# Kernel optimization log

Measured on AMD Instinct MI355X. Metric: run time of the kernel, lower is better.

The kernel has to match this reference:

```python
import jax, jax.numpy as jnp
import numpy as np

B, N, K = 2, 8192, 16
D_IN, D_OUT = 32, 128
EPS = 1e-5


def _bn(x, gamma, beta):
    # x: (B, C, L); BatchNorm1d training-mode stats over (B, L)
    mean = x.mean(axis=(0, 2), keepdims=True)
    var = x.var(axis=(0, 2), keepdims=True)
    return gamma[None, :, None] * (x - mean) * jax.lax.rsqrt(var + EPS) + beta[None, :, None]


def _shared_mlp(x, w, b, gamma, beta, act):
    # SharedMLP: 1x1 Conv1d (channel GEMM) + BN + activation. x: (B, Cin, L)
    y = jnp.einsum('oi,bil->bol', w, x) + b[None, :, None]
    return act(_bn(y, gamma, beta))


def _attentive_pool(x, w, b):
    # x: (B, C, N, K); per-(b,n,k) Linear over C, softmax over K, weighted sum over K
    scores = jnp.einsum('oc,bcnk->bonk', w, x) + b[None, :, None, None]
    scores = jax.nn.softmax(scores, axis=-1)
    return jnp.sum(scores * x, axis=-1)  # (B, C, N)  (torch keeps K=1 dim; squeezed by SharedMLP reshape)


def _knn(coords, k):
    # brute-force squared-L2 KNN excluding self (faiss IndexFlatL2 semantics)
    sq = jnp.sum(coords * coords, axis=-1)  # (B, N)
    d2 = sq[:, :, None] + sq[:, None, :] - 2.0 * jnp.einsum('bid,bjd->bij', coords, coords)
    n = coords.shape[1]
    d2 = jnp.where(jnp.eye(n, dtype=bool)[None], jnp.inf, d2)
    neg, idx = jax.lax.top_k(-d2, k)  # ascending squared distance
    return idx, jnp.maximum(-neg, 0.0)


def _lse(coords, features, idx, dist, w, b, gamma, beta):
    # LocalSpatialEncoding: gather neighbor coords, build 10-ch relative features, MLP, concat
    Bq, Nq, Kq = idx.shape
    neighbor = jax.vmap(lambda c, i: c[i])(coords, idx)  # (B, N, K, 3)
    center = jnp.broadcast_to(coords[:, :, None, :], neighbor.shape)
    rel = center - neighbor
    spatial = jnp.concatenate([center, neighbor, rel, dist[..., None]], axis=-1)  # (B, N, K, 10)
    spatial = spatial.transpose(0, 3, 1, 2).reshape(Bq, 10, Nq * Kq)
    sf = _shared_mlp(spatial, w, b, gamma, beta, jax.nn.relu).reshape(Bq, -1, Nq, Kq)
    feat = jnp.broadcast_to(features[..., None], (Bq, features.shape[1], Nq, Kq))
    return jnp.concatenate([sf, feat], axis=1)


def _forward(coords, features,
             mlp1_w, mlp1_b, mlp1_g, mlp1_bt,
             lse1_w, lse1_b, lse1_g, lse1_bt,
             mlpp1_w, mlpp1_b, mlpp1_g, mlpp1_bt,
             lse2_w, lse2_b, lse2_g, lse2_bt,
             mlp2_w, mlp2_b, mlp2_g, mlp2_bt,
             res_w, res_b, res_g, res_bt,
             pool1_w, pool1_b, pool2_w, pool2_b):
    # faiss output is detached in torch (numpy round-trip) -> stop_gradient
    idx, dist = _knn(jax.lax.stop_gradient(coords), K)
    lrelu02 = lambda v: jnp.where(v >= 0, v, 0.2 * v)   # LeakyReLU(0.2)
    lrelu01 = lambda v: jnp.where(v >= 0, v, 0.01 * v)  # default LeakyReLU
    x = _shared_mlp(features, mlp1_w, mlp1_b, mlp1_g, mlp1_bt, lrelu02)      # (B, 64, N)
    x = _lse(coords, x, idx, dist, lse1_w, lse1_b, lse1_g, lse1_bt)          # (B, 128, N, K)
    x = _attentive_pool(x, pool1_w, pool1_b)                                  # (B, 128, N)
    x = _shared_mlp(x, mlpp1_w, mlpp1_b, mlpp1_g, mlpp1_bt, jax.nn.relu)     # (B, 32, N)
    x = _lse(coords, x, idx, dist, lse2_w, lse2_b, lse2_g, lse2_bt)          # (B, 64, N, K)
    x = _attentive_pool(x, pool2_w, pool2_b)                                  # (B, 64, N)
    x_main = _shared_mlp(x, mlp2_w, mlp2_b, mlp2_g, mlp2_bt, jax.nn.relu)    # (B, 128, N)
    resid = _shared_mlp(features, res_w, res_b, res_g, res_bt, jax.nn.relu)  # (B, 128, N)
    return lrelu01(jnp.concatenate([x_main, resid], axis=1))                 # (B, 256, N)


def setup_inputs() -> dict:
    key = jax.random.key(0)
    ks = iter(jax.random.split(key, 64))

    def lin(ci, co):
        w = jax.random.normal(next(ks), (co, ci), jnp.float32) / np.float32(np.sqrt(ci))
        b = jax.random.normal(next(ks), (co,), jnp.float32) * 0.01
        return w, b

    inp = {}
    inp['coords'] = jax.random.normal(next(ks), (B, N, 3), jnp.float32)
    inp['features'] = jax.random.normal(next(ks), (B, D_IN, N), jnp.float32)
    for name, ci, co in [('mlp1', D_IN, D_OUT // 2), ('lse1', 10, D_OUT // 2),
                         ('mlpp1', D_OUT, D_OUT // 4), ('lse2', 10, D_OUT // 4),
                         ('mlp2', D_OUT // 2, D_OUT), ('res', D_IN, D_OUT)]:
        w, b = lin(ci, co)
        inp[name + '_w'], inp[name + '_b'] = w, b
        inp[name + '_g'] = jnp.ones((co,), jnp.float32)
        inp[name + '_bt'] = jnp.zeros((co,), jnp.float32)
    for name, c in [('pool1', D_OUT), ('pool2', D_OUT // 2)]:
        w, b = lin(c, c)
        inp[name + '_w'], inp[name + '_b'] = w, b
    return inp


def reference(coords, features,
              mlp1_w, mlp1_b, mlp1_g, mlp1_bt,
              lse1_w, lse1_b, lse1_g, lse1_bt,
              mlpp1_w, mlpp1_b, mlpp1_g, mlpp1_bt,
              lse2_w, lse2_b, lse2_g, lse2_bt,
              mlp2_w, mlp2_b, mlp2_g, mlp2_bt,
              res_w, res_b, res_g, res_bt,
              pool1_w, pool1_b, pool2_w, pool2_b):
    return _forward(coords, features,
                    mlp1_w, mlp1_b, mlp1_g, mlp1_bt,
                    lse1_w, lse1_b, lse1_g, lse1_bt,
                    mlpp1_w, mlpp1_b, mlpp1_g, mlpp1_bt,
                    lse2_w, lse2_b, lse2_g, lse2_bt,
                    mlp2_w, mlp2_b, mlp2_g, mlp2_bt,
                    res_w, res_b, res_g, res_bt,
                    pool1_w, pool1_b, pool2_w, pool2_b)
```

## Files before the change

kernel.cpp:

```cpp
#include <hip/hip_runtime.h>

static constexpr int N_ = 8192;
static constexpr int B_ = 2;
static constexpr int K_ = 16;

typedef __attribute__((ext_vector_type(8))) short bf16x8;
typedef __attribute__((ext_vector_type(4))) float f32x4;

__device__ __forceinline__ short f2bf(float f) {
  unsigned int u = __float_as_uint(f);
  unsigned int r = (u + 0x7FFFu + ((u >> 16) & 1u)) >> 16;
  return (short)r;
}
__device__ __forceinline__ float bf2f(short h) {
  return __uint_as_float(((unsigned int)(unsigned short)h) << 16);
}
__device__ __forceinline__ float dpp_shr1_f(float x) {
  return __uint_as_float((unsigned int)__builtin_amdgcn_update_dpp(
      0, (int)__float_as_uint(x), 0x111, 0xF, 0xF, true));
}
__device__ __forceinline__ int dpp_shr1_i(int x) {
  return __builtin_amdgcn_update_dpp(0, x, 0x111, 0xF, 0xF, true);
}
__device__ __forceinline__ float rdlane_f(float x, int l) {
  return __uint_as_float(__builtin_amdgcn_readlane(__float_as_uint(x), l));
}

__global__ __launch_bounds__(512) void knn_kernel(const float* __restrict__ coords,
                                                  int* __restrict__ oidx,
                                                  float* __restrict__ odist) {
  __shared__ float4 pts[2048];
  const int b = blockIdx.y;
  const int wv = threadIdx.x >> 6;
  const int lane = threadIdx.x & 63;
  const bool lpos = (lane != 0);
  const int q0 = blockIdx.x * 16 + wv * 2;
  const int q1 = q0 + 1;
  const float* cb = coords + (size_t)b * N_ * 3;
  const float qx0 = cb[q0 * 3 + 0], qy0 = cb[q0 * 3 + 1], qz0 = cb[q0 * 3 + 2];
  const float qx1 = cb[q1 * 3 + 0], qy1 = cb[q1 * 3 + 1], qz1 = cb[q1 * 3 + 2];
  const float qsq0 = __fadd_rn(__fadd_rn(__fmul_rn(qx0, qx0), __fmul_rn(qy0, qy0)), __fmul_rn(qz0, qz0));
  const float qsq1 = __fadd_rn(__fadd_rn(__fmul_rn(qx1, qx1), __fmul_rn(qy1, qy1)), __fmul_rn(qz1, qz1));
  float kd0 = INFINITY, kd1 = INFINITY;
  int ki0 = 0, ki1 = 0;
  float tau0 = INFINITY, tau1 = INFINITY;
  for (int t0 = 0; t0 < N_; t0 += 2048) {
    __syncthreads();
    for (int i = threadIdx.x; i < 2048; i += 512) {
      const int p = t0 + i;
      const float x = cb[p * 3 + 0], y = cb[p * 3 + 1], z = cb[p * 3 + 2];
      const float sq = __fadd_rn(__fadd_rn(__fmul_rn(x, x), __fmul_rn(y, y)), __fmul_rn(z, z));
      pts[i] = make_float4(x, y, z, sq);
    }
    __syncthreads();
    for (int s = 0; s < 2048; s += 64) {
      const float4 p = pts[s + lane];
      const int base = t0 + s;
      float d20, d21;
      {
        const float dot = __fadd_rn(__fadd_rn(__fmul_rn(qx0, p.x), __fmul_rn(qy0, p.y)), __fmul_rn(qz0, p.z));
        d20 = __fsub_rn(__fadd_rn(qsq0, p.w), __fmul_rn(2.0f, dot));
      }
      {
        const float dot = __fadd_rn(__fadd_rn(__fmul_rn(qx1, p.x), __fmul_rn(qy1, p.y)), __fmul_rn(qz1, p.z));
        d21 = __fsub_rn(__fadd_rn(qsq1, p.w), __fmul_rn(2.0f, dot));
      }
      unsigned long long m0 = __ballot(d20 < tau0);
      unsigned long long m1 = __ballot(d21 < tau1);
      if (base == (q0 & ~63)) m0 &= ~(1ull << (q0 & 63));
      if (base == (q1 & ~63)) m1 &= ~(1ull << (q1 & 63));
      while (m0) {
        const int src = __builtin_ctzll(m0);
        const float dc = rdlane_f(d20, src);
        const int jc = base + src;
        const float sd = dpp_shr1_f(kd0);
        const int si = dpp_shr1_i(ki0);
        const bool c1 = kd0 > dc;
        const bool c2 = lpos && (sd > dc);
        kd0 = c1 ? (c2 ? sd : dc) : kd0;
        ki0 = c1 ? (c2 ? si : jc) : ki0;
        m0 &= (m0 - 1);
        tau0 = rdlane_f(kd0, 15);
        m0 &= __ballot(d20 < tau0);
      }
      while (m1) {
        const int src = __builtin_ctzll(m1);
        const float dc = rdlane_f(d21, src);
        const int jc = base + src;
        const float sd = dpp_shr1_f(kd1);
        const int si = dpp_shr1_i(ki1);
        const bool c1 = kd1 > dc;
        const bool c2 = lpos && (sd > dc);
        kd1 = c1 ? (c2 ? sd : dc) : kd1;
        ki1 = c1 ? (c2 ? si : jc) : ki1;
        m1 &= (m1 - 1);
        tau1 = rdlane_f(kd1, 15);
        m1 &= __ballot(d21 < tau1);
      }
    }
  }
  if (lane < 16) {
    oidx[((size_t)b * N_ + q0) * K_ + lane] = ki0;
    odist[((size_t)b * N_ + q0) * K_ + lane] = fmaxf(kd0, 0.0f);
    oidx[((size_t)b * N_ + q1) * K_ + lane] = ki1;
    odist[((size_t)b * N_ + q1) * K_ + lane] = fmaxf(kd1, 0.0f);
  }
}

__device__ __forceinline__ float snn_get(const float* SNN, int a, int b) {
  const int i = a < b ? a : b, j = a < b ? b : a;
  return SNN[i == 0 ? j : (i == 1 ? 2 + j : 3 + j)];
}
__device__ __forceinline__ float mom_mean(int i, const float* C, const float* SN, float Sd) {
  if (i < 3) return 16.0f * C[i];
  if (i < 6) return SN[i - 3];
  if (i < 9) return 16.0f * C[i - 6] - SN[i - 6];
  return Sd;
}
__device__ __forceinline__ float mom_prod(int i, int j, const float* C, const float* SN,
                                          const float* SNN, float Sd, float Sdd, const float* SND) {
  const int ti = i < 3 ? 0 : (i < 6 ? 1 : (i < 9 ? 2 : 3));
  const int tj = j < 3 ? 0 : (j < 6 ? 1 : (j < 9 ? 2 : 3));
  const int a = (ti == 3) ? 0 : (i - ti * 3);
  const int bb = (tj == 3) ? 0 : (j - tj * 3);
  if (ti == 0 && tj == 0) return 16.0f * C[a] * C[bb];
  if (ti == 0 && tj == 1) return C[a] * SN[bb];
  if (ti == 0 && tj == 2) return C[a] * (16.0f * C[bb] - SN[bb]);
  if (ti == 0 && tj == 3) return C[a] * Sd;
  if (ti == 1 && tj == 1) return snn_get(SNN, a, bb);
  if (ti == 1 && tj == 2) return C[bb] * SN[a] - snn_get(SNN, a, bb);
  if (ti == 1 && tj == 3) return SND[a];
  if (ti == 2 && tj == 2) return 16.0f * C[a] * C[bb] - C[a] * SN[bb] - C[bb] * SN[a] + snn_get(SNN, a, bb);
  if (ti == 2 && tj == 3) return C[a] * Sd - SND[a];
  return Sdd;
}

__global__ __launch_bounds__(64) void moments_kernel(const float* __restrict__ coords,
                                                     const int* __restrict__ knn_i,
                                                     const float* __restrict__ knn_d,
                                                     double* __restrict__ mom) {
  const int t = blockIdx.x * 64 + threadIdx.x;
  const int b = t >> 13, n = t & (N_ - 1);
  const float* cb = coords + (size_t)b * N_ * 3;
  float C[3] = {cb[n * 3 + 0], cb[n * 3 + 1], cb[n * 3 + 2]};
  float SN[3] = {0.f, 0.f, 0.f}, SNN[6] = {0.f, 0.f, 0.f, 0.f, 0.f, 0.f};
  float SND[3] = {0.f, 0.f, 0.f}, Sd = 0.f, Sdd = 0.f;
  for (int k = 0; k < K_; ++k) {
    const int id = knn_i[(size_t)t * K_ + k];
    const float dd = knn_d[(size_t)t * K_ + k];
    const float nx = cb[id * 3 + 0], ny = cb[id * 3 + 1], nz = cb[id * 3 + 2];
    SN[0] += nx; SN[1] += ny; SN[2] += nz;
    SNN[0] += nx * nx; SNN[1] += nx * ny; SNN[2] += nx * nz;
    SNN[3] += ny * ny; SNN[4] += ny * nz; SNN[5] += nz * nz;
    Sd += dd; Sdd += dd * dd;
    SND[0] += nx * dd; SND[1] += ny * dd; SND[2] += nz * dd;
  }
  float m65[65];
  int e = 0;
#pragma unroll
  for (int i = 0; i < 10; ++i) m65[e++] = mom_mean(i, C, SN, Sd);
#pragma unroll
  for (int i = 0; i < 10; ++i)
#pragma unroll
    for (int j = i; j < 10; ++j) m65[e++] = mom_prod(i, j, C, SN, SNN, Sd, Sdd, SND);
#pragma unroll
  for (int q = 0; q < 65; ++q) {
    float v = m65[q];
#pragma unroll
    for (int off = 32; off > 0; off >>= 1) v += __shfl_xor(v, off);
    m65[q] = v;
  }
  __shared__ float buf[65];
  if (threadIdx.x == 0) {
#pragma unroll
    for (int q = 0; q < 65; ++q) buf[q] = m65[q];
  }
  __syncthreads();
  if (threadIdx.x < 64) atomicAdd(&mom[threadIdx.x], (double)buf[threadIdx.x]);
  if (threadIdx.x == 0) atomicAdd(&mom[64], (double)buf[64]);
}

template <int CI, int CO>
__device__ __forceinline__ void conv_frag_seg(const float* __restrict__ w, short* __restrict__ H,
                                              short* __restrict__ L, int tid, int nthr) {
  constexpr int NT = CO / 16;
  for (int i = tid; i < CI * CO; i += nthr) {
    const int j = i & 7, l = (i >> 3) & 63, tmp = i >> 9;
    const int tt = tmp % NT, cc = tmp / NT;
    const int c = cc * 32 + (l >> 4) * 8 + j;
    const int o = tt * 16 + (l & 15);
    const float v = w[o * CI + c];
    const short h = f2bf(v);
    H[i] = h;
    L[i] = f2bf(v - bf2f(h));
  }
}

__global__ __launch_bounds__(256) void convert_kernel(
    const float* __restrict__ pw1, const float* __restrict__ pw2,
    short* __restrict__ wB1, short* __restrict__ wB2,
    const float* __restrict__ wm1, short* __restrict__ f1H, short* __restrict__ f1L,
    const float* __restrict__ wmp, short* __restrict__ f2H, short* __restrict__ f2L,
    const float* __restrict__ wm2, short* __restrict__ f3H, short* __restrict__ f3L,
    const float* __restrict__ wrs, short* __restrict__ fRH, short* __restrict__ fRL) {
  const int blk = blockIdx.x;
  if (blk < 8) {
    const int tid = blk * 256 + threadIdx.x;
    for (int i = tid; i < 128 * 128; i += 2048) wB1[i] = f2bf(pw1[i]);
  } else if (blk < 10) {
    const int tid = (blk - 8) * 256 + threadIdx.x;
    for (int i = tid; i < 64 * 64; i += 512) wB2[i] = f2bf(pw2[i]);
  } else if (blk < 12) {
    conv_frag_seg<32, 64>(wm1, f1H, f1L, (blk - 10) * 256 + threadIdx.x, 512);
  } else if (blk < 16) {
    conv_frag_seg<128, 32>(wmp, f2H, f2L, (blk - 12) * 256 + threadIdx.x, 1024);
  } else if (blk < 24) {
    conv_frag_seg<64, 128>(wm2, f3H, f3L, (blk - 16) * 256 + threadIdx.x, 2048);
  } else {
    conv_frag_seg<32, 128>(wrs, fRH, fRL, (blk - 24) * 256 + threadIdx.x, 1024);
  }
}

__global__ void setup_kernel(const double* __restrict__ mom,
                             const float* __restrict__ w1, const float* __restrict__ b1,
                             const float* __restrict__ g1, const float* __restrict__ t1,
                             const float* __restrict__ w2, const float* __restrict__ b2,
                             const float* __restrict__ g2, const float* __restrict__ t2,
                             float* __restrict__ w1f, float* __restrict__ b1f,
                             float* __restrict__ w2f, float* __restrict__ b2f) {
  const int t = threadIdx.x;
  __shared__ double mu[10];
  __shared__ double S[10][10];
  const double cnt = (double)B_ * N_ * K_;
  if (t < 10) mu[t] = mom[t] / cnt;
  if (t < 55) {
    int e = t, i = 0;
    while (e >= 10 - i) { e -= 10 - i; ++i; }
    const int j = i + e;
    const double v = mom[10 + t] / cnt;
    S[i][j] = v;
    S[j][i] = v;
  }
  __syncthreads();
  const float *w, *bias, *gg, *bt;
  float *wf, *bf;
  int c;
  if (t < 64) { w = w1; bias = b1; gg = g1; bt = t1; wf = w1f; bf = b1f; c = t; }
  else if (t < 96) { w = w2; bias = b2; gg = g2; bt = t2; wf = w2f; bf = b2f; c = t - 64; }
  else return;
  double wd[10];
#pragma unroll
  for (int d = 0; d < 10; ++d) wd[d] = (double)w[c * 10 + d];
  const double cbv = (double)bias[c];
  double mz = cbv;
  for (int d = 0; d < 10; ++d) mz += wd[d] * mu[d];
  double e2 = cbv * cbv;
  for (int d = 0; d < 10; ++d) e2 += 2.0 * cbv * wd[d] * mu[d];
  for (int d = 0; d < 10; ++d)
    for (int e = 0; e < 10; ++e) e2 += wd[d] * wd[e] * S[d][e];
  const double var = e2 - mz * mz;
  const double a = (double)gg[c] / sqrt(var + 1e-5);
  const double shift = (double)bt[c] - a * mz;
#pragma unroll
  for (int d = 0; d < 10; ++d) wf[c * 10 + d] = (float)(a * wd[d]);
  bf[c] = (float)(a * cbv + shift);
}

template <int CI, int CO, bool ROWMAJ>
__global__ __launch_bounds__(256) void gemm_mfma_kernel(const float* __restrict__ in,
                                                        const short* __restrict__ fragH,
                                                        const short* __restrict__ fragL,
                                                        const float* __restrict__ bias,
                                                        float* __restrict__ out,
                                                        double* __restrict__ sacc) {
  constexpr int NT = CO / 16;
  constexpr int NC = CI / 32;
  __shared__ float part[4][CO][2];
  const int wv = threadIdx.x >> 6, l = threadIdx.x & 63;
  const int col = l & 15, quad = l >> 4;
  const int p0 = blockIdx.x * 64 + wv * 16;
  const int pt = p0 + col;
  f32x4 d[NT];
#pragma unroll
  for (int t = 0; t < NT; ++t) {
    const float bv = bias[t * 16 + col];
    d[t][0] = bv; d[t][1] = bv; d[t][2] = bv; d[t][3] = bv;
  }
#pragma unroll
  for (int cc = 0; cc < NC; ++cc) {
    float xv[8];
    if (ROWMAJ) {
      const float* ip = in + (size_t)pt * CI + cc * 32 + quad * 8;
      *(float4*)&xv[0] = *(const float4*)ip;
      *(float4*)&xv[4] = *(const float4*)(ip + 4);
    } else {
      const int b = pt >> 13, n = pt & (N_ - 1);
      const float* ip = in + ((size_t)b * CI + cc * 32 + quad * 8) * N_ + n;
#pragma unroll
      for (int j = 0; j < 8; ++j) xv[j] = ip[(size_t)j * N_];
    }
    union { bf16x8 v; short u[8]; } AH, AL;
#pragma unroll
    for (int j = 0; j < 8; ++j) {
      const short h = f2bf(xv[j]);
      AH.u[j] = h;
      AL.u[j] = f2bf(xv[j] - bf2f(h));
    }
#pragma unroll
    for (int t = 0; t < NT; ++t) {
      const size_t fo = ((size_t)(cc * NT + t) * 64 + l) * 8;
      const bf16x8 BH = *(const bf16x8*)(fragH + fo);
      const bf16x8 BL = *(const bf16x8*)(fragL + fo);
      d[t] = __builtin_amdgcn_mfma_f32_16x16x32_bf16(AH.v, BH, d[t], 0, 0, 0);
      d[t] = __builtin_amdgcn_mfma_f32_16x16x32_bf16(AH.v, BL, d[t], 0, 0, 0);
      d[t] = __builtin_amdgcn_mfma_f32_16x16x32_bf16(AL.v, BH, d[t], 0, 0, 0);
    }
  }
#pragma unroll
  for (int t = 0; t < NT; ++t) {
#pragma unroll
    for (int r = 0; r < 4; ++r)
      out[(size_t)(p0 + quad * 4 + r) * CO + t * 16 + col] = d[t][r];
    float s1 = d[t][0] + d[t][1] + d[t][2] + d[t][3];
    float s2 = d[t][0] * d[t][0] + d[t][1] * d[t][1] + d[t][2] * d[t][2] + d[t][3] * d[t][3];
    s1 += __shfl_xor(s1, 16); s1 += __shfl_xor(s1, 32);
    s2 += __shfl_xor(s2, 16); s2 += __shfl_xor(s2, 32);
    if (quad == 0) { part[wv][t * 16 + col][0] = s1; part[wv][t * 16 + col][1] = s2; }
  }
  __syncthreads();
  if (threadIdx.x < CO) {
    const int o = threadIdx.x;
    atomicAdd(&sacc[o], (double)(part[0][o][0] + part[1][o][0] + part[2][o][0] + part[3][o][0]));
    atomicAdd(&sacc[CO + o], (double)(part[0][o][1] + part[1][o][1] + part[2][o][1] + part[3][o][1]));
  }
}

template <int CSF, int CF>
__global__ __launch_bounds__(256) void pool_kernel(
    const float* __restrict__ coords, const int* __restrict__ knn_i, const float* __restrict__ knn_d,
    const float* __restrict__ wlse, const float* __restrict__ blse,
    const float* __restrict__ feat, const double* __restrict__ sfe,
    const float* __restrict__ gfe, const float* __restrict__ tfe,
    const float slope,
    const short* __restrict__ wB, const float* __restrict__ pb,
    float* __restrict__ out) {
  constexpr int C = CSF + CF;
  constexpr int CP = C + 4;
  constexpr int NT = C / 16;
  constexpr int NC = C / 32;
  __shared__ float xcat[4][16][CP];
  __shared__ float sp[4][10][16];
  const int g = threadIdx.x >> 6;
  const int l = threadIdx.x & 63;
  const int quad = l >> 4, col = l & 15;
  const int pid = blockIdx.x * 4 + g;
  const int b = pid >> 13, n = pid & (N_ - 1);
  const float* cb = coords + (size_t)b * N_ * 3;

  if (l < 16) {
    const int id = knn_i[(size_t)pid * K_ + l];
    const float dd = knn_d[(size_t)pid * K_ + l];
    const float cx = cb[n * 3 + 0], cy = cb[n * 3 + 1], cz = cb[n * 3 + 2];
    const float nx = cb[id * 3 + 0], ny = cb[id * 3 + 1], nz = cb[id * 3 + 2];
    sp[g][0][l] = cx; sp[g][1][l] = cy; sp[g][2][l] = cz;
    sp[g][3][l] = nx; sp[g][4][l] = ny; sp[g][5][l] = nz;
    sp[g][6][l] = cx - nx; sp[g][7][l] = cy - ny; sp[g][8][l] = cz - nz;
    sp[g][9][l] = dd;
  }
  if (l < CF) {
    const double cnt = (double)(B_ * N_);
    const double mean = sfe[l] / cnt;
    const double var = sfe[CF + l] / cnt - mean * mean;
    const double av = (double)gfe[l] / sqrt(var + 1e-5);
    const float af = (float)av;
    const float bfv = (float)((double)tfe[l] - av * mean);
    float v = feat[(size_t)pid * CF + l];
    v = af * v + bfv;
    v = (v >= 0.0f) ? v : slope * v;
#pragma unroll
    for (int j = 0; j < 16; ++j) xcat[g][j][CSF + l] = v;
  }
  __syncthreads();
  if (l < CSF) {
    float z[16];
    const float bz = blse[l];
#pragma unroll
    for (int j = 0; j < 16; ++j) z[j] = bz;
#pragma unroll
    for (int d = 0; d < 10; ++d) {
      const float wv = wlse[l * 10 + d];
      const float4* sr = (const float4*)&sp[g][d][0];
      const float4 s0 = sr[0], s1 = sr[1], s2 = sr[2], s3 = sr[3];
      z[0] += wv * s0.x; z[1] += wv * s0.y; z[2] += wv * s0.z; z[3] += wv * s0.w;
      z[4] += wv * s1.x; z[5] += wv * s1.y; z[6] += wv * s1.z; z[7] += wv * s1.w;
      z[8] += wv * s2.x; z[9] += wv * s2.y; z[10] += wv * s2.z; z[11] += wv * s2.w;
      z[12] += wv * s3.x; z[13] += wv * s3.y; z[14] += wv * s3.z; z[15] += wv * s3.w;
    }
#pragma unroll
    for (int j = 0; j < 16; ++j) xcat[g][j][l] = fmaxf(z[j], 0.0f);
  }
  __syncthreads();
  f32x4 d[NT];
#pragma unroll
  for (int t = 0; t < NT; ++t) {
    const float pbv = pb[t * 16 + col];
    d[t][0] = pbv; d[t][1] = pbv; d[t][2] = pbv; d[t][3] = pbv;
  }
#pragma unroll
  for (int cc = 0; cc < NC; ++cc) {
    const float* xr = &xcat[g][col][cc * 32 + quad * 8];
    const float4 xa = *(const float4*)xr;
    const float4 xb = *(const float4*)(xr + 4);
    union { bf16x8 v; short u[8]; } A;
    A.u[0] = f2bf(xa.x); A.u[1] = f2bf(xa.y); A.u[2] = f2bf(xa.z); A.u[3] = f2bf(xa.w);
    A.u[4] = f2bf(xb.x); A.u[5] = f2bf(xb.y); A.u[6] = f2bf(xb.z); A.u[7] = f2bf(xb.w);
#pragma unroll
    for (int t = 0; t < NT; ++t) {
      const bf16x8 Bv = *(const bf16x8*)(wB + (size_t)(t * 16 + col) * C + cc * 32 + quad * 8);
      d[t] = __builtin_amdgcn_mfma_f32_16x16x32_bf16(A.v, Bv, d[t], 0, 0, 0);
    }
  }
#pragma unroll
  for (int t = 0; t < NT; ++t) {
    float mx = fmaxf(fmaxf(d[t][0], d[t][1]), fmaxf(d[t][2], d[t][3]));
    mx = fmaxf(mx, __shfl_xor(mx, 16));
    mx = fmaxf(mx, __shfl_xor(mx, 32));
    float e0 = __expf(d[t][0] - mx), e1 = __expf(d[t][1] - mx);
    float e2 = __expf(d[t][2] - mx), e3 = __expf(d[t][3] - mx);
    float s = e0 + e1 + e2 + e3;
    s += __shfl_xor(s, 16);
    s += __shfl_xor(s, 32);
    const int o = t * 16 + col;
    float part = e0 * xcat[g][quad * 4 + 0][o] + e1 * xcat[g][quad * 4 + 1][o] +
                 e2 * xcat[g][quad * 4 + 2][o] + e3 * xcat[g][quad * 4 + 3][o];
    part += __shfl_xor(part, 16);
    part += __shfl_xor(part, 32);
    if (quad == 0) out[(size_t)pid * C + o] = part / s;
  }
}

__global__ __launch_bounds__(256) void final_kernel(const float* __restrict__ y3,
                                                    const float* __restrict__ yr,
                                                    const double* __restrict__ s3,
                                                    const float* __restrict__ g3, const float* __restrict__ t3,
                                                    const double* __restrict__ sr,
                                                    const float* __restrict__ gr, const float* __restrict__ tr,
                                                    float* __restrict__ out) {
  __shared__ float tile[256 * 17];
  const int blk = blockIdx.x;
  const int b = blk >> 9;
  const int n0 = (blk & 511) << 4;
  const int c = threadIdx.x;
  const float* src;
  const double* sa;
  const float *gp, *tp;
  int cc;
  if (c < 128) { src = y3; sa = s3; gp = g3; tp = t3; cc = c; }
  else { src = yr; sa = sr; gp = gr; tp = tr; cc = c - 128; }
  const double cnt = (double)(B_ * N_);
  const double mean = sa[cc] / cnt;
  const double var = sa[128 + cc] / cnt - mean * mean;
  const double avd = (double)gp[cc] / sqrt(var + 1e-5);
  const float av = (float)avd;
  const float bv = (float)((double)tp[cc] - avd * mean);
#pragma unroll
  for (int nl = 0; nl < 16; ++nl) {
    const float x = av * src[((size_t)(b * N_ + n0 + nl)) * 128 + cc] + bv;
    tile[c * 17 + nl] = fmaxf(x, 0.0f);
  }
  __syncthreads();
  const int np = c & 15, grp = c >> 4;
#pragma unroll
  for (int j = 0; j < 16; ++j) {
    const int c2 = grp * 16 + j;
    out[((size_t)(b * 256 + c2)) * N_ + n0 + np] = tile[c2 * 17 + np];
  }
}

extern "C" void kernel_launch(void* const* d_in, const int* in_sizes, int n_in,
                              void* d_out, int out_size, void* d_ws, size_t ws_size,
                              hipStream_t stream) {
  (void)in_sizes; (void)n_in; (void)out_size; (void)ws_size;
  const float* coords   = (const float*)d_in[0];
  const float* features = (const float*)d_in[1];
  const float* mlp1_w = (const float*)d_in[2];
  const float* mlp1_b = (const float*)d_in[3];
  const float* mlp1_g = (const float*)d_in[4];
  const float* mlp1_t = (const float*)d_in[5];
  const float* lse1_w = (const float*)d_in[6];
  const float* lse1_b = (const float*)d_in[7];
  const float* lse1_g = (const float*)d_in[8];
  const float* lse1_t = (const float*)d_in[9];
  const float* mlpp1_w = (const float*)d_in[10];
  const float* mlpp1_b = (const float*)d_in[11];
  const float* mlpp1_g = (const float*)d_in[12];
  const float* mlpp1_t = (const float*)d_in[13];
  const float* lse2_w = (const float*)d_in[14];
  const float* lse2_b = (const float*)d_in[15];
  const float* lse2_g = (const float*)d_in[16];
  const float* lse2_t = (const float*)d_in[17];
  const float* mlp2_w = (const float*)d_in[18];
  const float* mlp2_b = (const float*)d_in[19];
  const float* mlp2_g = (const float*)d_in[20];
  const float* mlp2_t = (const float*)d_in[21];
  const float* res_w = (const float*)d_in[22];
  const float* res_b = (const float*)d_in[23];
  const float* res_g = (const float*)d_in[24];
  const float* res_t = (const float*)d_in[25];
  const float* pool1_w = (const float*)d_in[26];
  const float* pool1_b = (const float*)d_in[27];
  const float* pool2_w = (const float*)d_in[28];
  const float* pool2_b = (const float*)d_in[29];

  float* wsf = (float*)d_ws;
  int* knn_i = (int*)d_ws;
  float* knn_d = wsf + 262144;
  float* y1 = wsf + 524288;
  float* pooled1 = wsf + 1572864;
  float* y2 = wsf + 3670016;
  float* pooled2 = wsf + 4194304;
  float* y3 = wsf + 5242880;
  float* yr = wsf + 7340032;
  double* dacc = (double*)(wsf + 9437184);
  double* mom = dacc;
  double* sacc_mlp1 = dacc + 65;
  double* sacc_mlpp1 = dacc + 193;
  double* sacc_mlp2 = dacc + 257;
  double* sacc_res = dacc + 513;
  float* fpar = wsf + 9437184 + 1600;
  float* w1f = fpar;
  float* b1f = w1f + 640;
  float* w2f = b1f + 64;
  float* b2f = w2f + 320;
  short* wB1 = (short*)(b2f + 32);
  short* wB2 = wB1 + 16384;
  short* f1H = wB2 + 4096;
  short* f1L = f1H + 2048;
  short* f2H = f1L + 2048;
  short* f2L = f2H + 4096;
  short* f3H = f2L + 4096;
  short* f3L = f3H + 8192;
  short* fRH = f3L + 8192;
  short* fRL = fRH + 4096;

  hipMemsetAsync(dacc, 0, 769 * sizeof(double), stream);
  knn_kernel<<<dim3(N_ / 16, B_), 512, 0, stream>>>(coords, knn_i, knn_d);
  convert_kernel<<<28, 256, 0, stream>>>(pool1_w, pool2_w, wB1, wB2,
                                         mlp1_w, f1H, f1L, mlpp1_w, f2H, f2L,
                                         mlp2_w, f3H, f3L, res_w, fRH, fRL);
  moments_kernel<<<256, 64, 0, stream>>>(coords, knn_i, knn_d, mom);
  setup_kernel<<<1, 128, 0, stream>>>(mom, lse1_w, lse1_b, lse1_g, lse1_t,
                                      lse2_w, lse2_b, lse2_g, lse2_t,
                                      w1f, b1f, w2f, b2f);
  gemm_mfma_kernel<32, 64, false><<<256, 256, 0, stream>>>(features, f1H, f1L, mlp1_b, y1, sacc_mlp1);
  pool_kernel<64, 64><<<B_ * N_ / 4, 256, 0, stream>>>(
      coords, knn_i, knn_d, w1f, b1f, y1, sacc_mlp1, mlp1_g, mlp1_t, 0.2f, wB1, pool1_b, pooled1);
  gemm_mfma_kernel<128, 32, true><<<256, 256, 0, stream>>>(pooled1, f2H, f2L, mlpp1_b, y2, sacc_mlpp1);
  pool_kernel<32, 32><<<B_ * N_ / 4, 256, 0, stream>>>(
      coords, knn_i, knn_d, w2f, b2f, y2, sacc_mlpp1, mlpp1_g, mlpp1_t, 0.0f, wB2, pool2_b, pooled2);
  gemm_mfma_kernel<64, 128, true><<<256, 256, 0, stream>>>(pooled2, f3H, f3L, mlp2_b, y3, sacc_mlp2);
  gemm_mfma_kernel<32, 128, false><<<256, 256, 0, stream>>>(features, fRH, fRL, res_b, yr, sacc_res);
  final_kernel<<<B_ * 512, 256, 0, stream>>>(y3, yr, sacc_mlp2, mlp2_g, mlp2_t,
                                             sacc_res, res_g, res_t, (float*)d_out);
}
```

Baseline: 434.9 us.

## Fold relative-coord LSE weights algebraically, vectorize KNN tile load, batch tau refresh

The setup kernel folds the center, neighbor and relative-coordinate weights of the 10-channel LSE conv into 7 effective weights plus bias. The pool kernel can then compute the per-point center term once and do 4 FMAs per neighbor instead of 10. The KNN kernel now loads coordinate tiles as float4 (three float4 per thread covering four points) and refreshes the top-k threshold once per 64-candidate chunk instead of after every insertion. That last part may insert more candidates that the stale threshold would have pruned, and the folded weights change float rounding slightly.

```diff
diff --git a/kernel.cpp b/kernel.cpp
--- a/kernel.cpp
+++ b/kernel.cpp
@@ -46,11 +46,21 @@
   float tau0 = INFINITY, tau1 = INFINITY;
   for (int t0 = 0; t0 < N_; t0 += 2048) {
     __syncthreads();
-    for (int i = threadIdx.x; i < 2048; i += 512) {
-      const int p = t0 + i;
-      const float x = cb[p * 3 + 0], y = cb[p * 3 + 1], z = cb[p * 3 + 2];
-      const float sq = __fadd_rn(__fadd_rn(__fmul_rn(x, x), __fmul_rn(y, y)), __fmul_rn(z, z));
-      pts[i] = make_float4(x, y, z, sq);
+    {
+      const float4* cb4 = (const float4*)(cb + (size_t)t0 * 3);
+      const int t = threadIdx.x;
+      const float4 a = cb4[3 * t + 0];
+      const float4 bb = cb4[3 * t + 1];
+      const float4 c = cb4[3 * t + 2];
+      const float px[4] = {a.x, a.w, bb.z, c.y};
+      const float py[4] = {a.y, bb.x, bb.w, c.z};
+      const float pz[4] = {a.z, bb.y, c.x, c.w};
+#pragma unroll
+      for (int u = 0; u < 4; ++u) {
+        const float sq = __fadd_rn(__fadd_rn(__fmul_rn(px[u], px[u]), __fmul_rn(py[u], py[u])),
+                                   __fmul_rn(pz[u], pz[u]));
+        pts[4 * t + u] = make_float4(px[u], py[u], pz[u], sq);
+      }
     }
     __syncthreads();
     for (int s = 0; s < 2048; s += 64) {
@@ -69,33 +79,35 @@
       unsigned long long m1 = __ballot(d21 < tau1);
       if (base == (q0 & ~63)) m0 &= ~(1ull << (q0 & 63));
       if (base == (q1 & ~63)) m1 &= ~(1ull << (q1 & 63));
-      while (m0) {
-        const int src = __builtin_ctzll(m0);
-        const float dc = rdlane_f(d20, src);
-        const int jc = base + src;
-        const float sd = dpp_shr1_f(kd0);
-        const int si = dpp_shr1_i(ki0);
-        const bool c1 = kd0 > dc;
-        const bool c2 = lpos && (sd > dc);
-        kd0 = c1 ? (c2 ? sd : dc) : kd0;
-        ki0 = c1 ? (c2 ? si : jc) : ki0;
-        m0 &= (m0 - 1);
+      if (m0) {
+        do {
+          const int src = __builtin_ctzll(m0);
+          const float dc = rdlane_f(d20, src);
+          const int jc = base + src;
+          const float sd = dpp_shr1_f(kd0);
+          const int si = dpp_shr1_i(ki0);
+          const bool c1 = kd0 > dc;
+          const bool c2 = lpos && (sd > dc);
+          kd0 = c1 ? (c2 ? sd : dc) : kd0;
+          ki0 = c1 ? (c2 ? si : jc) : ki0;
+          m0 &= (m0 - 1);
+        } while (m0);
         tau0 = rdlane_f(kd0, 15);
-        m0 &= __ballot(d20 < tau0);
       }
-      while (m1) {
-        const int src = __builtin_ctzll(m1);
-        const float dc = rdlane_f(d21, src);
-        const int jc = base + src;
-        const float sd = dpp_shr1_f(kd1);
-        const int si = dpp_shr1_i(ki1);
-        const bool c1 = kd1 > dc;
-        const bool c2 = lpos && (sd > dc);
-        kd1 = c1 ? (c2 ? sd : dc) : kd1;
-        ki1 = c1 ? (c2 ? si : jc) : ki1;
-        m1 &= (m1 - 1);
+      if (m1) {
+        do {
+          const int src = __builtin_ctzll(m1);
+          const float dc = rdlane_f(d21, src);
+          const int jc = base + src;
+          const float sd = dpp_shr1_f(kd1);
+          const int si = dpp_shr1_i(ki1);
+          const bool c1 = kd1 > dc;
+          const bool c2 = lpos && (sd > dc);
+          kd1 = c1 ? (c2 ? sd : dc) : kd1;
+          ki1 = c1 ? (c2 ? si : jc) : ki1;
+          m1 &= (m1 - 1);
+        } while (m1);
         tau1 = rdlane_f(kd1, 15);
-        m1 &= __ballot(d21 < tau1);
       }
     }
   }
@@ -226,8 +238,7 @@
                              const float* __restrict__ g1, const float* __restrict__ t1,
                              const float* __restrict__ w2, const float* __restrict__ b2,
                              const float* __restrict__ g2, const float* __restrict__ t2,
-                             float* __restrict__ w1f, float* __restrict__ b1f,
-                             float* __restrict__ w2f, float* __restrict__ b2f) {
+                             float* __restrict__ w1f8, float* __restrict__ w2f8) {
   const int t = threadIdx.x;
   __shared__ double mu[10];
   __shared__ double S[10][10];
@@ -243,10 +254,10 @@
   }
   __syncthreads();
   const float *w, *bias, *gg, *bt;
-  float *wf, *bf;
+  float *wf;
   int c;
-  if (t < 64) { w = w1; bias = b1; gg = g1; bt = t1; wf = w1f; bf = b1f; c = t; }
-  else if (t < 96) { w = w2; bias = b2; gg = g2; bt = t2; wf = w2f; bf = b2f; c = t - 64; }
+  if (t < 64) { w = w1; bias = b1; gg = g1; bt = t1; wf = w1f8; c = t; }
+  else if (t < 96) { w = w2; bias = b2; gg = g2; bt = t2; wf = w2f8; c = t - 64; }
   else return;
   double wd[10];
 #pragma unroll
@@ -261,9 +272,14 @@
   const double var = e2 - mz * mz;
   const double a = (double)gg[c] / sqrt(var + 1e-5);
   const double shift = (double)bt[c] - a * mz;
-#pragma unroll
-  for (int d = 0; d < 10; ++d) wf[c * 10 + d] = (float)(a * wd[d]);
-  bf[c] = (float)(a * cbv + shift);
+  wf[c * 8 + 0] = (float)(a * (wd[0] + wd[6]));
+  wf[c * 8 + 1] = (float)(a * (wd[1] + wd[7]));
+  wf[c * 8 + 2] = (float)(a * (wd[2] + wd[8]));
+  wf[c * 8 + 3] = (float)(a * (wd[3] - wd[6]));
+  wf[c * 8 + 4] = (float)(a * (wd[4] - wd[7]));
+  wf[c * 8 + 5] = (float)(a * (wd[5] - wd[8]));
+  wf[c * 8 + 6] = (float)(a * wd[9]);
+  wf[c * 8 + 7] = (float)(a * cbv + shift);
 }
 
 template <int CI, int CO, bool ROWMAJ>
@@ -338,7 +354,7 @@
 template <int CSF, int CF>
 __global__ __launch_bounds__(256) void pool_kernel(
     const float* __restrict__ coords, const int* __restrict__ knn_i, const float* __restrict__ knn_d,
-    const float* __restrict__ wlse, const float* __restrict__ blse,
+    const float* __restrict__ w8,
     const float* __restrict__ feat, const double* __restrict__ sfe,
     const float* __restrict__ gfe, const float* __restrict__ tfe,
     const float slope,
@@ -349,7 +365,8 @@
   constexpr int NT = C / 16;
   constexpr int NC = C / 32;
   __shared__ float xcat[4][16][CP];
-  __shared__ float sp[4][10][16];
+  __shared__ float4 sp4[4][16];
+  __shared__ float4 spc[4];
   const int g = threadIdx.x >> 6;
   const int l = threadIdx.x & 63;
   const int quad = l >> 4, col = l & 15;
@@ -360,12 +377,9 @@
   if (l < 16) {
     const int id = knn_i[(size_t)pid * K_ + l];
     const float dd = knn_d[(size_t)pid * K_ + l];
-    const float cx = cb[n * 3 + 0], cy = cb[n * 3 + 1], cz = cb[n * 3 + 2];
     const float nx = cb[id * 3 + 0], ny = cb[id * 3 + 1], nz = cb[id * 3 + 2];
-    sp[g][0][l] = cx; sp[g][1][l] = cy; sp[g][2][l] = cz;
-    sp[g][3][l] = nx; sp[g][4][l] = ny; sp[g][5][l] = nz;
-    sp[g][6][l] = cx - nx; sp[g][7][l] = cy - ny; sp[g][8][l] = cz - nz;
-    sp[g][9][l] = dd;
+    sp4[g][l] = make_float4(nx, ny, nz, dd);
+    if (l == 0) spc[g] = make_float4(cb[n * 3 + 0], cb[n * 3 + 1], cb[n * 3 + 2], 0.0f);
   }
   if (l < CF) {
     const double cnt = (double)(B_ * N_);
@@ -382,22 +396,16 @@
   }
   __syncthreads();
   if (l < CSF) {
-    float z[16];
-    const float bz = blse[l];
-#pragma unroll
-    for (int j = 0; j < 16; ++j) z[j] = bz;
-#pragma unroll
-    for (int d = 0; d < 10; ++d) {
-      const float wv = wlse[l * 10 + d];
-      const float4* sr = (const float4*)&sp[g][d][0];
-      const float4 s0 = sr[0], s1 = sr[1], s2 = sr[2], s3 = sr[3];
-      z[0] += wv * s0.x; z[1] += wv * s0.y; z[2] += wv * s0.z; z[3] += wv * s0.w;
-      z[4] += wv * s1.x; z[5] += wv * s1.y; z[6] += wv * s1.z; z[7] += wv * s1.w;
-      z[8] += wv * s2.x; z[9] += wv * s2.y; z[10] += wv * s2.z; z[11] += wv * s2.w;
-      z[12] += wv * s3.x; z[13] += wv * s3.y; z[14] += wv * s3.z; z[15] += wv * s3.w;
-    }
-#pragma unroll
-    for (int j = 0; j < 16; ++j) xcat[g][j][l] = fmaxf(z[j], 0.0f);
+    const float4 wA = *(const float4*)(w8 + l * 8);
+    const float4 wBv = *(const float4*)(w8 + l * 8 + 4);
+    const float4 C4 = spc[g];
+    const float tterm = wBv.w + wA.x * C4.x + wA.y * C4.y + wA.z * C4.z;
+#pragma unroll
+    for (int k = 0; k < 16; ++k) {
+      const float4 nk = sp4[g][k];
+      const float z = tterm + wA.w * nk.x + wBv.x * nk.y + wBv.y * nk.z + wBv.z * nk.w;
+      xcat[g][k][l] = fmaxf(z, 0.0f);
+    }
   }
   __syncthreads();
   f32x4 d[NT];
@@ -528,11 +536,9 @@
   double* sacc_mlp2 = dacc + 257;
   double* sacc_res = dacc + 513;
   float* fpar = wsf + 9437184 + 1600;
-  float* w1f = fpar;
-  float* b1f = w1f + 640;
-  float* w2f = b1f + 64;
-  float* b2f = w2f + 320;
-  short* wB1 = (short*)(b2f + 32);
+  float* w1f8 = fpar;
+  float* w2f8 = w1f8 + 512;
+  short* wB1 = (short*)(w2f8 + 256);
   short* wB2 = wB1 + 16384;
   short* f1H = wB2 + 4096;
   short* f1L = f1H + 2048;
@@ -550,14 +556,13 @@
                                          mlp2_w, f3H, f3L, res_w, fRH, fRL);
   moments_kernel<<<256, 64, 0, stream>>>(coords, knn_i, knn_d, mom);
   setup_kernel<<<1, 128, 0, stream>>>(mom, lse1_w, lse1_b, lse1_g, lse1_t,
-                                      lse2_w, lse2_b, lse2_g, lse2_t,
-                                      w1f, b1f, w2f, b2f);
+                                      lse2_w, lse2_b, lse2_g, lse2_t, w1f8, w2f8);
   gemm_mfma_kernel<32, 64, false><<<256, 256, 0, stream>>>(features, f1H, f1L, mlp1_b, y1, sacc_mlp1);
   pool_kernel<64, 64><<<B_ * N_ / 4, 256, 0, stream>>>(
-      coords, knn_i, knn_d, w1f, b1f, y1, sacc_mlp1, mlp1_g, mlp1_t, 0.2f, wB1, pool1_b, pooled1);
+      coords, knn_i, knn_d, w1f8, y1, sacc_mlp1, mlp1_g, mlp1_t, 0.2f, wB1, pool1_b, pooled1);
   gemm_mfma_kernel<128, 32, true><<<256, 256, 0, stream>>>(pooled1, f2H, f2L, mlpp1_b, y2, sacc_mlpp1);
   pool_kernel<32, 32><<<B_ * N_ / 4, 256, 0, stream>>>(
-      coords, knn_i, knn_d, w2f, b2f, y2, sacc_mlpp1, mlpp1_g, mlpp1_t, 0.0f, wB2, pool2_b, pooled2);
+      coords, knn_i, knn_d, w2f8, y2, sacc_mlpp1, mlpp1_g, mlpp1_t, 0.0f, wB2, pool2_b, pooled2);
   gemm_mfma_kernel<64, 128, true><<<256, 256, 0, stream>>>(pooled2, f3H, f3L, mlp2_b, y3, sacc_mlp2);
   gemm_mfma_kernel<32, 128, false><<<256, 256, 0, stream>>>(features, fRH, fRL, res_b, yr, sacc_res);
   final_kernel<<<B_ * 512, 256, 0, stream>>>(y3, yr, sacc_mlp2, mlp2_g, mlp2_t,
```

Result: no change. 433.4 us (-0.3%).
